# Performance work log

Hardware: AMD Instinct MI355X
Metric: run time of the kernel (lower is better)

Reference implementation:

```python
import jax, jax.numpy as jnp
import numpy as np

B, SQ, SD, H = 64, 64, 512, 128


def setup_inputs() -> dict:
    key = jax.random.key(0)
    k1, k2, k3, k4, k5 = jax.random.split(key, 5)
    q = jax.random.normal(k1, (B, SQ, H), dtype=jnp.float32)
    d_pos = jax.random.normal(k2, (B, SD, H), dtype=jnp.float32)
    d_neg = jax.random.normal(k3, (B, SD, H), dtype=jnp.float32)
    mask_pos = jax.random.randint(k4, (B, SD), 0, 2, dtype=jnp.int32).at[:, 0].set(1)
    mask_neg = jax.random.randint(k5, (B, SD), 0, 2, dtype=jnp.int32).at[:, 0].set(1)
    return {"q": q, "d_pos": d_pos, "d_neg": d_neg,
            "mask_pos": mask_pos, "mask_neg": mask_neg}


def _colbert_maxsim(q, d, mask):
    # q: [a, s, h], d: [b, t, h], mask: [b, t] -> scores [a, b]
    simis = jnp.einsum('ash,bth->abst', q, d)            # [a, b, s, t]
    simis = jnp.where(mask[None, :, None, :] == 0, -jnp.inf, simis)
    return simis.max(axis=3).sum(axis=2)                 # max over t, sum over s


def reference(q, d_pos, d_neg, mask_pos, mask_neg):
    # Concatenate pos and in-batch-negative score blocks -> [B, 2B]
    distances = jnp.concatenate(
        [_colbert_maxsim(q, d_pos, mask_pos),
         _colbert_maxsim(q, d_neg, mask_neg)], axis=1)
    labels = jnp.arange(q.shape[0])
    logp = jax.nn.log_softmax(distances, axis=1)
    loss = -jnp.take_along_axis(logp, labels[:, None], axis=1).mean()
    return loss
```

## Files before the change

### kernel.cpp

```cpp
#include <hip/hip_runtime.h>
#include <hip/hip_bf16.h>
#include <math.h>
#include <stdint.h>

#define BB 64
#define SQN 64
#define SDN 512
#define HH 128

typedef __attribute__((ext_vector_type(8))) short bf16x8;
typedef __attribute__((ext_vector_type(16))) float f32x16;

__device__ __forceinline__ short f2bf(float f) {
  union { float f; unsigned u; } x; x.f = f;
  unsigned r = x.u + 0x7fffu + ((x.u >> 16) & 1u);
  return (short)(r >> 16);
}

__device__ __forceinline__ void gl_lds16(const short* g, short* l) {
  __builtin_amdgcn_global_load_lds(
      (const __attribute__((address_space(1))) unsigned int*)g,
      (__attribute__((address_space(3))) unsigned int*)l, 16, 0, 0);
}

__global__ __launch_bounds__(256)
void convert_kernel(const float* __restrict__ q, const float* __restrict__ dp,
                    const float* __restrict__ dn,
                    const int* __restrict__ mp, const int* __restrict__ mn,
                    short* __restrict__ oq, short* __restrict__ od,
                    int* __restrict__ nchunks, int* __restrict__ counter) {
  const int tid = threadIdx.x;
  if (blockIdx.x < 2048) {
    const int gid = blockIdx.x;
    const int bs  = gid >> 4;
    const int sub = gid & 15;
    const int side = bs >> 6, b = bs & 63;
    const int* mask = side ? mn : mp;
    const float* srcmat = side ? dn : dp;
    __shared__ int perm_lds[SDN];
    __shared__ int pad_s;
    if (tid < 64) {
      int run = 0;
      #pragma unroll
      for (int it = 0; it < SDN / 64; ++it) {
        int t = it * 64 + tid;
        int m = mask[b * SDN + t];
        unsigned long long bal = __ballot(m != 0);
        int pos = run + __popcll(bal & ((1ull << tid) - 1ull));
        if (m) perm_lds[pos] = t;
        run += (int)__popcll(bal);
      }
      int pad = (run + 127) & ~127;
      for (int j = run + tid; j < pad; j += 64) perm_lds[j] = -1;
      if (tid == 0) {
        pad_s = pad;
        if (sub == 0) nchunks[bs] = pad >> 7;
      }
    }
    __syncthreads();
    const int pad = pad_s;
    const int l32 = tid & 31;
    #pragma unroll
    for (int p = 0; p < 4; ++p) {
      int j = sub * 32 + p * 8 + (tid >> 5);
      if (j < pad) {
        int src_t = perm_lds[j];
        float4 v = make_float4(0.f, 0.f, 0.f, 0.f);
        if (src_t >= 0)
          v = ((const float4*)(srcmat + ((size_t)b * SDN + src_t) * HH))[l32];
        short4 o; o.x = f2bf(v.x); o.y = f2bf(v.y); o.z = f2bf(v.z); o.w = f2bf(v.w);
        *(short4*)&od[((size_t)bs * SDN + j) * HH + l32 * 4] = o;
      }
    }
  } else {
    if (blockIdx.x == 2048 && tid == 0) counter[0] = 0;
    const int bq = blockIdx.x - 2048;
    #pragma unroll
    for (int it = 0; it < 16; ++it) {
      int i = bq * 4096 + it * 256 + tid;
      float4 v = ((const float4*)q)[i];
      short4 o; o.x = f2bf(v.x); o.y = f2bf(v.y); o.z = f2bf(v.z); o.w = f2bf(v.w);
      *(short4*)&oq[i * 4] = o;
    }
  }
}

__global__ __launch_bounds__(256, 2)
void maxsim_kernel(const short* __restrict__ qb,
                   const short* __restrict__ dc,
                   const int* __restrict__ nchunks,
                   float* __restrict__ scores,
                   int* __restrict__ counter,
                   float* __restrict__ out) {
  const int aslc = blockIdx.x;
  const int bs0  = blockIdx.y * 2;

  __shared__ __align__(16) short d_lds[2][128 * 128];
  __shared__ int islast_s;

  const int tid = threadIdx.x;
  const int ln  = tid & 63;
  const int w   = tid >> 6;
  const int l31 = ln & 31;
  const int kh  = ln >> 5;
  const int a0  = aslc * 8 + w * 2;

  int nchv[2];
  nchv[0] = nchunks[bs0];
  nchv[1] = nchunks[bs0 + 1];

  bf16x8 qfrag[2][2][8];
  #pragma unroll
  for (int al = 0; al < 2; ++al)
    #pragma unroll
    for (int half = 0; half < 2; ++half) {
      const short* qrow = qb + ((size_t)(a0 + al) * SQN + half * 32 + l31) * HH + kh * 8;
      #pragma unroll
      for (int kc = 0; kc < 8; ++kc)
        qfrag[al][half][kc] = *(const bf16x8*)(qrow + kc * 16);
    }

  float rmax[2][2] = {{0.f, 0.f}, {0.f, 0.f}};

  {
    const short* dsrc = dc + (size_t)bs0 * SDN * HH;
    #pragma unroll
    for (int it = 0; it < 8; ++it) {
      int f = it * 256 + tid;
      int row = f >> 4;
      int c = (f & 15) ^ (row & 15);
      gl_lds16(&dsrc[row * HH + c * 8], &d_lds[0][(it * 256 + w * 64) * 8]);
    }
  }
  __syncthreads();

  int bi = 0, tc = 0, buf = 0;
  for (;;) {
    int nbi = bi, ntc = tc + 1;
    if (ntc == nchv[bi]) { ntc = 0; nbi = bi + 1; }
    const bool hn = (nbi < 2);

    if (hn) {
      const short* dsrc = dc + ((size_t)(bs0 + nbi) * SDN + ntc * 128) * HH;
      short* dst = &d_lds[buf ^ 1][0];
      #pragma unroll
      for (int it = 0; it < 8; ++it) {
        int f = it * 256 + tid;
        int row = f >> 4;
        int c = (f & 15) ^ (row & 15);
        gl_lds16(&dsrc[row * HH + c * 8], &dst[(it * 256 + w * 64) * 8]);
      }
    }

    const short* bufp = &d_lds[buf][0];
    #pragma unroll
    for (int tt = 0; tt < 4; ++tt) {
      int trow = tt * 32 + l31;
      int tm = trow & 15;
      const short* bbase = &bufp[trow * HH];
      f32x16 acc00 = {0,0,0,0,0,0,0,0,0,0,0,0,0,0,0,0};
      f32x16 acc01 = {0,0,0,0,0,0,0,0,0,0,0,0,0,0,0,0};
      f32x16 acc10 = {0,0,0,0,0,0,0,0,0,0,0,0,0,0,0,0};
      f32x16 acc11 = {0,0,0,0,0,0,0,0,0,0,0,0,0,0,0,0};
      #pragma unroll
      for (int kc = 0; kc < 8; ++kc) {
        int c = (kc * 2 + kh) ^ tm;
        bf16x8 dfrag = *(const bf16x8*)&bbase[c * 8];
        acc00 = __builtin_amdgcn_mfma_f32_32x32x16_bf16(dfrag, qfrag[0][0][kc], acc00, 0, 0, 0);
        acc01 = __builtin_amdgcn_mfma_f32_32x32x16_bf16(dfrag, qfrag[0][1][kc], acc01, 0, 0, 0);
        acc10 = __builtin_amdgcn_mfma_f32_32x32x16_bf16(dfrag, qfrag[1][0][kc], acc10, 0, 0, 0);
        acc11 = __builtin_amdgcn_mfma_f32_32x32x16_bf16(dfrag, qfrag[1][1][kc], acc11, 0, 0, 0);
      }
      float m00 = acc00[0], m01 = acc01[0], m10 = acc10[0], m11 = acc11[0];
      #pragma unroll
      for (int r = 1; r < 16; ++r) {
        m00 = fmaxf(m00, acc00[r]);
        m01 = fmaxf(m01, acc01[r]);
        m10 = fmaxf(m10, acc10[r]);
        m11 = fmaxf(m11, acc11[r]);
      }
      rmax[0][0] = fmaxf(rmax[0][0], m00);
      rmax[0][1] = fmaxf(rmax[0][1], m01);
      rmax[1][0] = fmaxf(rmax[1][0], m10);
      rmax[1][1] = fmaxf(rmax[1][1], m11);
    }

    if (ntc == 0) {
      #pragma unroll
      for (int al = 0; al < 2; ++al) {
        float v0 = fmaxf(rmax[al][0], __shfl_xor(rmax[al][0], 32));
        float v1 = fmaxf(rmax[al][1], __shfl_xor(rmax[al][1], 32));
        float s = v0 + v1;
        s += __shfl_xor(s, 1);  s += __shfl_xor(s, 2);  s += __shfl_xor(s, 4);
        s += __shfl_xor(s, 8);  s += __shfl_xor(s, 16);
        if (ln == 0) scores[(size_t)(a0 + al) * (2 * BB) + bs0 + bi] = s;
        rmax[al][0] = 0.f; rmax[al][1] = 0.f;
      }
    }

    __syncthreads();
    if (!hn) break;
    bi = nbi; tc = ntc; buf ^= 1;
  }

  __syncthreads();
  if (tid == 0) {
    __threadfence();
    int old = atomicAdd(counter, 1);
    islast_s = (old == 511);
  }
  __syncthreads();
  if (!islast_s) return;
  __threadfence();

  __shared__ float part[4];
  float acc = 0.f;
  for (int i = 0; i < 16; ++i) {
    int r = w * 16 + i;
    float v0 = scores[r * 128 + ln];
    float v1 = scores[r * 128 + 64 + ln];
    float mx = fmaxf(v0, v1);
    #pragma unroll
    for (int off = 32; off >= 1; off >>= 1) mx = fmaxf(mx, __shfl_xor(mx, off));
    float e = __expf(v0 - mx) + __expf(v1 - mx);
    #pragma unroll
    for (int off = 32; off >= 1; off >>= 1) e += __shfl_xor(e, off);
    float lse = mx + __logf(e);
    float diag = __shfl(v0, r);
    acc += lse - diag;
  }
  if (ln == 0) part[w] = acc;
  __syncthreads();
  if (tid == 0)
    out[0] = (part[0] + part[1] + part[2] + part[3]) * (1.0f / 64.0f);
}

extern "C" void kernel_launch(void* const* d_in, const int* in_sizes, int n_in,
                              void* d_out, int out_size, void* d_ws, size_t ws_size,
                              hipStream_t stream) {
  const float* q        = (const float*)d_in[0];
  const float* d_pos    = (const float*)d_in[1];
  const float* d_neg    = (const float*)d_in[2];
  const int*   mask_pos = (const int*)d_in[3];
  const int*   mask_neg = (const int*)d_in[4];

  short* q_bf = (short*)d_ws;
  short* d_c  = q_bf + (size_t)BB * SQN * HH;
  int*   nchunks = (int*)(d_c + (size_t)2 * BB * SDN * HH);
  float* scores  = (float*)(nchunks + 128);
  int*   counter = (int*)(scores + BB * 2 * BB);

  convert_kernel<<<2080, 256, 0, stream>>>(q, d_pos, d_neg, mask_pos, mask_neg,
                                           q_bf, d_c, nchunks, counter);

  dim3 grid(8 , 64 );
  maxsim_kernel<<<grid, 256, 0, stream>>>(q_bf, d_c, nchunks, scores,
                                          counter, (float*)d_out);
}
```

Measured before the change: 146.9 us.

## Use 64-row doc chunks, one query per wave, four docs per block

```diff
diff --git a/kernel.cpp b/kernel.cpp
--- a/kernel.cpp
+++ b/kernel.cpp
@@ -50,11 +50,11 @@
         if (m) perm_lds[pos] = t;
         run += (int)__popcll(bal);
       }
-      int pad = (run + 127) & ~127;
+      int pad = (run + 63) & ~63;
       for (int j = run + tid; j < pad; j += 64) perm_lds[j] = -1;
       if (tid == 0) {
         pad_s = pad;
-        if (sub == 0) nchunks[bs] = pad >> 7;
+        if (sub == 0) nchunks[bs] = pad >> 6;
       }
     }
     __syncthreads();
@@ -85,7 +85,7 @@
   }
 }
 
-__global__ __launch_bounds__(256, 2)
+__global__ __launch_bounds__(256, 3)
 void maxsim_kernel(const short* __restrict__ qb,
                    const short* __restrict__ dc,
                    const int* __restrict__ nchunks,
@@ -93,9 +93,9 @@
                    int* __restrict__ counter,
                    float* __restrict__ out) {
   const int aslc = blockIdx.x;
-  const int bs0  = blockIdx.y * 2;
-
-  __shared__ __align__(16) short d_lds[2][128 * 128];
+  const int bs0  = blockIdx.y * 4;
+
+  __shared__ __align__(16) short d_lds[2][64 * 128];
   __shared__ int islast_s;
 
   const int tid = threadIdx.x;
@@ -103,29 +103,27 @@
   const int w   = tid >> 6;
   const int l31 = ln & 31;
   const int kh  = ln >> 5;
-  const int a0  = aslc * 8 + w * 2;
-
-  int nchv[2];
-  nchv[0] = nchunks[bs0];
-  nchv[1] = nchunks[bs0 + 1];
-
-  bf16x8 qfrag[2][2][8];
+  const int a   = aslc * 4 + w;
+
+  int nchv[4];
   #pragma unroll
-  for (int al = 0; al < 2; ++al)
-    #pragma unroll
-    for (int half = 0; half < 2; ++half) {
-      const short* qrow = qb + ((size_t)(a0 + al) * SQN + half * 32 + l31) * HH + kh * 8;
-      #pragma unroll
-      for (int kc = 0; kc < 8; ++kc)
-        qfrag[al][half][kc] = *(const bf16x8*)(qrow + kc * 16);
-    }
-
-  float rmax[2][2] = {{0.f, 0.f}, {0.f, 0.f}};
+  for (int i = 0; i < 4; ++i) nchv[i] = nchunks[bs0 + i];
+
+  bf16x8 qfrag[2][8];
+  #pragma unroll
+  for (int half = 0; half < 2; ++half) {
+    const short* qrow = qb + ((size_t)a * SQN + half * 32 + l31) * HH + kh * 8;
+    #pragma unroll
+    for (int kc = 0; kc < 8; ++kc)
+      qfrag[half][kc] = *(const bf16x8*)(qrow + kc * 16);
+  }
+
+  float rmaxh[2] = {0.f, 0.f};
 
   {
     const short* dsrc = dc + (size_t)bs0 * SDN * HH;
     #pragma unroll
-    for (int it = 0; it < 8; ++it) {
+    for (int it = 0; it < 4; ++it) {
       int f = it * 256 + tid;
       int row = f >> 4;
       int c = (f & 15) ^ (row & 15);
@@ -138,13 +136,13 @@
   for (;;) {
     int nbi = bi, ntc = tc + 1;
     if (ntc == nchv[bi]) { ntc = 0; nbi = bi + 1; }
-    const bool hn = (nbi < 2);
+    const bool hn = (nbi < 4);
 
     if (hn) {
-      const short* dsrc = dc + ((size_t)(bs0 + nbi) * SDN + ntc * 128) * HH;
+      const short* dsrc = dc + ((size_t)(bs0 + nbi) * SDN + ntc * 64) * HH;
       short* dst = &d_lds[buf ^ 1][0];
       #pragma unroll
-      for (int it = 0; it < 8; ++it) {
+      for (int it = 0; it < 4; ++it) {
         int f = it * 256 + tid;
         int row = f >> 4;
         int c = (f & 15) ^ (row & 15);
@@ -154,48 +152,37 @@
 
     const short* bufp = &d_lds[buf][0];
     #pragma unroll
-    for (int tt = 0; tt < 4; ++tt) {
+    for (int tt = 0; tt < 2; ++tt) {
       int trow = tt * 32 + l31;
       int tm = trow & 15;
       const short* bbase = &bufp[trow * HH];
-      f32x16 acc00 = {0,0,0,0,0,0,0,0,0,0,0,0,0,0,0,0};
-      f32x16 acc01 = {0,0,0,0,0,0,0,0,0,0,0,0,0,0,0,0};
-      f32x16 acc10 = {0,0,0,0,0,0,0,0,0,0,0,0,0,0,0,0};
-      f32x16 acc11 = {0,0,0,0,0,0,0,0,0,0,0,0,0,0,0,0};
+      f32x16 acc0 = {0,0,0,0,0,0,0,0,0,0,0,0,0,0,0,0};
+      f32x16 acc1 = {0,0,0,0,0,0,0,0,0,0,0,0,0,0,0,0};
       #pragma unroll
       for (int kc = 0; kc < 8; ++kc) {
         int c = (kc * 2 + kh) ^ tm;
         bf16x8 dfrag = *(const bf16x8*)&bbase[c * 8];
-        acc00 = __builtin_amdgcn_mfma_f32_32x32x16_bf16(dfrag, qfrag[0][0][kc], acc00, 0, 0, 0);
-        acc01 = __builtin_amdgcn_mfma_f32_32x32x16_bf16(dfrag, qfrag[0][1][kc], acc01, 0, 0, 0);
-        acc10 = __builtin_amdgcn_mfma_f32_32x32x16_bf16(dfrag, qfrag[1][0][kc], acc10, 0, 0, 0);
-        acc11 = __builtin_amdgcn_mfma_f32_32x32x16_bf16(dfrag, qfrag[1][1][kc], acc11, 0, 0, 0);
-      }
-      float m00 = acc00[0], m01 = acc01[0], m10 = acc10[0], m11 = acc11[0];
+        acc0 = __builtin_amdgcn_mfma_f32_32x32x16_bf16(dfrag, qfrag[0][kc], acc0, 0, 0, 0);
+        acc1 = __builtin_amdgcn_mfma_f32_32x32x16_bf16(dfrag, qfrag[1][kc], acc1, 0, 0, 0);
+      }
+      float m0 = acc0[0], m1 = acc1[0];
       #pragma unroll
       for (int r = 1; r < 16; ++r) {
-        m00 = fmaxf(m00, acc00[r]);
-        m01 = fmaxf(m01, acc01[r]);
-        m10 = fmaxf(m10, acc10[r]);
-        m11 = fmaxf(m11, acc11[r]);
-      }
-      rmax[0][0] = fmaxf(rmax[0][0], m00);
-      rmax[0][1] = fmaxf(rmax[0][1], m01);
-      rmax[1][0] = fmaxf(rmax[1][0], m10);
-      rmax[1][1] = fmaxf(rmax[1][1], m11);
+        m0 = fmaxf(m0, acc0[r]);
+        m1 = fmaxf(m1, acc1[r]);
+      }
+      rmaxh[0] = fmaxf(rmaxh[0], m0);
+      rmaxh[1] = fmaxf(rmaxh[1], m1);
     }
 
     if (ntc == 0) {
-      #pragma unroll
-      for (int al = 0; al < 2; ++al) {
-        float v0 = fmaxf(rmax[al][0], __shfl_xor(rmax[al][0], 32));
-        float v1 = fmaxf(rmax[al][1], __shfl_xor(rmax[al][1], 32));
-        float s = v0 + v1;
-        s += __shfl_xor(s, 1);  s += __shfl_xor(s, 2);  s += __shfl_xor(s, 4);
-        s += __shfl_xor(s, 8);  s += __shfl_xor(s, 16);
-        if (ln == 0) scores[(size_t)(a0 + al) * (2 * BB) + bs0 + bi] = s;
-        rmax[al][0] = 0.f; rmax[al][1] = 0.f;
-      }
+      float v0 = fmaxf(rmaxh[0], __shfl_xor(rmaxh[0], 32));
+      float v1 = fmaxf(rmaxh[1], __shfl_xor(rmaxh[1], 32));
+      float s = v0 + v1;
+      s += __shfl_xor(s, 1);  s += __shfl_xor(s, 2);  s += __shfl_xor(s, 4);
+      s += __shfl_xor(s, 8);  s += __shfl_xor(s, 16);
+      if (ln == 0) scores[(size_t)a * (2 * BB) + bs0 + bi] = s;
+      rmaxh[0] = 0.f; rmaxh[1] = 0.f;
     }
 
     __syncthreads();
@@ -253,7 +240,7 @@
   convert_kernel<<<2080, 256, 0, stream>>>(q, d_pos, d_neg, mask_pos, mask_neg,
                                            q_bf, d_c, nchunks, counter);
 
-  dim3 grid(8 , 64 );
+  dim3 grid(16 , 32 );
   maxsim_kernel<<<grid, 256, 0, stream>>>(q_bf, d_c, nchunks, scores,
                                           counter, (float*)d_out);
 }
```

Measured after the change: 144.6 us. Within noise of the previous version (-1.6%).
